# Kernel optimization log

Hardware: AMD Instinct MI355X
Metric: run time of the kernel (lower is better)

## Reference

```python
import jax, jax.numpy as jnp
import numpy as np

N_HEAD = 12
TOP_M = 16
MIN_SIZE = 2
MAX_SIZE = 8
ALPHA = 1.0
EPS = 1e-6

# Note: in the torch source, minimize_det=True and minimize_det=False select the
# identical subset (the sign flip in the score is exactly undone by flipping the
# comparisons), so we implement the single equivalent rule: maximize
# s = -log(det(K_S K_S^T) + 1e-6) / |S|**alpha.

def _token(qi, i, k_all, v_all):
    """Greedy DPP subset selection for one query token i. qi:[d], k_all/v_all:[T,d]."""
    T, d = k_all.shape
    slots = jnp.arange(MAX_SIZE)
    sim = k_all @ qi
    sim = jnp.where(jnp.arange(T) <= i, sim, -jnp.inf)  # causal mask
    vals, topidx = jax.lax.top_k(sim, TOP_M)
    avail0 = jnp.isfinite(vals) & (topidx != i)  # i is removed from candidates
    k_cand = k_all[topidx]                        # [M,d]
    cand_norm = jnp.sum(k_cand * k_cand, axis=-1)  # [M]
    ki = k_all[i]
    sel0 = jnp.zeros((MAX_SIZE,), jnp.int32).at[0].set(i.astype(jnp.int32))
    s0 = jax.lax.stop_gradient(-jnp.log(jnp.dot(ki, ki) + EPS))  # |S|=1 => size^alpha=1

    def body(state, _):
        sel, count, cur_s, avail, done = state
        # E: selected key vectors in slots < count, zeros elsewhere
        E = jnp.where((slots < count)[:, None], k_all[sel], 0.0)  # [S,d]
        G0 = E @ E.T                                              # [S,S]
        cross = k_cand @ E.T  # [M,S]; column `count` is 0 since that E row is 0
        u = (slots == count).astype(E.dtype)  # one-hot insertion slot
        # Gram of S u {c} for every candidate c, identity-padded beyond slot count
        grams = (G0[None]
                 + u[None, :, None] * cross[:, None, :]
                 + cross[:, :, None] * u[None, None, :]
                 + cand_norm[:, None, None] * (u[:, None] * u[None, :])[None])
        grams = grams + jnp.diag(jnp.where(slots > count, 1.0, 0.0))[None]
        det = jnp.linalg.det(grams.astype(jnp.float32))  # [M]
        s = -jnp.log(det + EPS) / (count + 1).astype(jnp.float32) ** ALPHA
        s = jax.lax.stop_gradient(jnp.where(avail, s, -jnp.inf))
        best = jnp.argmax(s)
        best_s = s[best]
        accept = (~done) & jnp.any(avail) & ((best_s > cur_s) | (count < MIN_SIZE))
        sel = jnp.where(accept & (slots == count), topidx[best].astype(jnp.int32), sel)
        avail = avail & ~(accept & (jnp.arange(TOP_M) == best))
        cur_s = jnp.where(accept, best_s, cur_s)
        count = count + accept.astype(count.dtype)
        done = done | ~accept
        return (sel, count, cur_s, avail, done), None

    init = (sel0, jnp.int32(1), s0, avail0, jnp.bool_(False))
    (sel, count, _, _, _), _ = jax.lax.scan(body, init, None, length=MAX_SIZE - 1)
    w = (slots < count).astype(v_all.dtype)
    return (v_all[sel] * w[:, None]).sum(0) / count.astype(v_all.dtype)

_tokens = jax.vmap(_token, in_axes=(0, 0, None, None))  # over T

def _head(qh, kh, vh):
    return _tokens(qh, jnp.arange(qh.shape[0]), kh, vh)

_attn = jax.vmap(jax.vmap(_head))  # over B, H

def _forward(x, W_attn, b_attn, W_proj, b_proj):
    B, T, C = x.shape
    hs = C // N_HEAD
    qkv = x @ W_attn + b_attn
    q, k, v = jnp.split(qkv, 3, axis=-1)
    q = q.reshape(B, T, N_HEAD, hs).transpose(0, 2, 1, 3)
    k = k.reshape(B, T, N_HEAD, hs).transpose(0, 2, 1, 3)
    v = v.reshape(B, T, N_HEAD, hs).transpose(0, 2, 1, 3)
    y = _attn(q, k, v)  # [B,H,T,hs]
    y = y.transpose(0, 2, 1, 3).reshape(B, T, C)
    return y @ W_proj + b_proj  # dropout=0.0 (eval)

def setup_inputs():
    key = jax.random.key(0)
    ks = jax.random.split(key, 3)
    B, T, C = 4, 512, 768
    return {
        "x": jax.random.normal(ks[0], (B, T, C), jnp.float32),
        "W_attn": jax.random.normal(ks[1], (C, 3 * C), jnp.float32) * 0.02,
        "b_attn": jnp.zeros((3 * C,), jnp.float32),
        "W_proj": jax.random.normal(ks[2], (C, C), jnp.float32) * 0.02,
        "b_proj": jnp.zeros((C,), jnp.float32),
    }

def reference(x, W_attn, b_attn, W_proj, b_proj):
    return _forward(x, W_attn, b_attn, W_proj, b_proj)
```

## Files before the change

### kernel.cpp

```cpp
#include <hip/hip_runtime.h>
#include <math.h>

constexpr int Bc = 4, Tc = 512, Cc = 768, Hc = 12, HSc = 64;
constexpr int QKVN = 3 * Cc;
constexpr double EPSd = 1e-6;

typedef unsigned short u16;
typedef __attribute__((ext_vector_type(8))) short short8;
typedef __attribute__((ext_vector_type(4))) float f32x4;

__device__ __forceinline__ u16 f2bf(float x) {
  unsigned u = __float_as_uint(x);
  return (u16)((u + 0x7FFFu + ((u >> 16) & 1u)) >> 16);
}
__device__ __forceinline__ float bf2f(u16 h) {
  return __uint_as_float((unsigned)h << 16);
}

__device__ __forceinline__ void gload16(const u16* g, u16* l) {
  __builtin_amdgcn_global_load_lds(
      (const __attribute__((address_space(1))) void*)g,
      (__attribute__((address_space(3))) void*)l, 16, 0, 0);
}

#define WAITVM0 asm volatile("s_waitcnt vmcnt(0)" ::: "memory")

__global__ void __launch_bounds__(256) convsplit3(
    const float* __restrict__ in, u16* __restrict__ H, u16* __restrict__ M,
    u16* __restrict__ L) {
  const int i = blockIdx.x * 256 + threadIdx.x;
  const float4 v = ((const float4*)in)[i];
  const float x[4] = {v.x, v.y, v.z, v.w};
  ushort4 hv, mv, lv;
  u16* hp = (u16*)&hv; u16* mp = (u16*)&mv; u16* lp = (u16*)&lv;
#pragma unroll
  for (int c = 0; c < 4; ++c) {
    const u16 h = f2bf(x[c]);
    const float r1 = x[c] - bf2f(h);
    const u16 m = f2bf(r1);
    const u16 l = f2bf(r1 - bf2f(m));
    hp[c] = h; mp[c] = m; lp[c] = l;
  }
  ((ushort4*)H)[i] = hv;
  ((ushort4*)M)[i] = mv;
  ((ushort4*)L)[i] = lv;
}

__global__ void __launch_bounds__(256) convsplit3_t(
    const float* __restrict__ W, u16* __restrict__ Th, u16* __restrict__ Tm,
    u16* __restrict__ Tl, int K, int Nn) {
  __shared__ float t[64][65];
  const int k0 = blockIdx.x * 64, n0 = blockIdx.y * 64;
#pragma unroll
  for (int u = 0; u < 16; ++u) {
    const int idx = u * 256 + threadIdx.x;
    const int r = idx >> 6, c = idx & 63;
    t[r][c] = W[(size_t)(k0 + r) * Nn + n0 + c];
  }
  __syncthreads();
#pragma unroll
  for (int u = 0; u < 16; ++u) {
    const int idx = u * 256 + threadIdx.x;
    const int n = idx >> 6, k = idx & 63;
    const float x = t[k][n];
    const u16 h = f2bf(x);
    const float r1 = x - bf2f(h);
    const u16 m = f2bf(r1);
    const u16 l = f2bf(r1 - bf2f(m));
    Th[(size_t)(n0 + n) * K + k0 + k] = h;
    Tm[(size_t)(n0 + n) * K + k0 + k] = m;
    Tl[(size_t)(n0 + n) * K + k0 + k] = l;
  }
}

template <bool WRITE_PARTIAL, int PLANES>
__global__ void __launch_bounds__(256, 3) gemm_mfma3(
    const u16* __restrict__ A, const u16* __restrict__ B,
    const float* __restrict__ bias, float* __restrict__ outp,
    int N, int kPerSplit, int strideA, int strideB) {
  __shared__ __align__(16) u16 AsF[2][PLANES * 64 * 32];
  __shared__ __align__(16) u16 BsF[2][PLANES * 64 * 32];
  const int tid = threadIdx.x;
  const int wid = tid >> 6;
  const int lane = tid & 63;
  const int lm = lane & 15, kg = lane >> 4;
  const int wr = wid >> 1, wc = wid & 1;
  const int rb = blockIdx.x * 64;
  const int cb = blockIdx.y * 64;
  const int kBeg = blockIdx.z * kPerSplit;

  const int trow = tid >> 2;
  const int tc4 = tid & 3;
  const int krot = ((tc4 - (trow >> 1)) & 3) * 8;
  const int sLds = tid * 8;
  int aOff = (rb + trow) * 768 + kBeg + krot;
  int bOff = (cb + trow) * 768 + kBeg + krot;

  f32x4 acc[2][2];
#pragma unroll
  for (int mf = 0; mf < 2; ++mf)
#pragma unroll
    for (int nf = 0; nf < 2; ++nf) acc[mf][nf] = (f32x4){0.f, 0.f, 0.f, 0.f};

  const int nIter = kPerSplit / 32;
  const int ckA = ((kg + (lm >> 1)) & 3) * 8;

  auto waitN = [&]() {
    if constexpr (PLANES == 3) {
      asm volatile("s_waitcnt vmcnt(6)" ::: "memory");
    } else {
      asm volatile("s_waitcnt vmcnt(4)" ::: "memory");
    }
  };
  auto stage = [&](int buf) {
#pragma unroll
    for (int p = 0; p < PLANES; ++p) {
      gload16(A + (size_t)p * strideA + aOff, &AsF[buf][p * 2048 + sLds]);
      gload16(B + (size_t)p * strideB + bOff, &BsF[buf][p * 2048 + sLds]);
    }
    aOff += 32; bOff += 32;
  };
  auto compute = [&](int buf) {
    short8 ah[2], am[2], al[2];
#pragma unroll
    for (int mf = 0; mf < 2; ++mf) {
      const int ro = (wr * 32 + mf * 16 + lm) * 32 + ckA;
      ah[mf] = *(const short8*)&AsF[buf][ro];
      am[mf] = *(const short8*)&AsF[buf][2048 + ro];
      if constexpr (PLANES == 3) al[mf] = *(const short8*)&AsF[buf][4096 + ro];
    }
#pragma unroll
    for (int nf = 0; nf < 2; ++nf) {
      const int co = (wc * 32 + nf * 16 + lm) * 32 + ckA;
      const short8 bh = *(const short8*)&BsF[buf][co];
      const short8 bm = *(const short8*)&BsF[buf][2048 + co];
      short8 bl;
      if constexpr (PLANES == 3) bl = *(const short8*)&BsF[buf][4096 + co];
#pragma unroll
      for (int mf = 0; mf < 2; ++mf) {
        if constexpr (PLANES == 3) {
          acc[mf][nf] = __builtin_amdgcn_mfma_f32_16x16x32_bf16(
              al[mf], bh, acc[mf][nf], 0, 0, 0);
          acc[mf][nf] = __builtin_amdgcn_mfma_f32_16x16x32_bf16(
              ah[mf], bl, acc[mf][nf], 0, 0, 0);
          acc[mf][nf] = __builtin_amdgcn_mfma_f32_16x16x32_bf16(
              am[mf], bm, acc[mf][nf], 0, 0, 0);
        }
        acc[mf][nf] = __builtin_amdgcn_mfma_f32_16x16x32_bf16(
            am[mf], bh, acc[mf][nf], 0, 0, 0);
        acc[mf][nf] = __builtin_amdgcn_mfma_f32_16x16x32_bf16(
            ah[mf], bm, acc[mf][nf], 0, 0, 0);
        acc[mf][nf] = __builtin_amdgcn_mfma_f32_16x16x32_bf16(
            ah[mf], bh, acc[mf][nf], 0, 0, 0);
      }
    }
  };

  stage(0);
  stage(1);
  for (int t = 0; t < nIter; t += 2) {
    if (t + 1 < nIter) { waitN(); } else { WAITVM0; }
    __builtin_amdgcn_s_barrier();
    compute(0);
    __builtin_amdgcn_s_barrier();
    if (t + 2 < nIter) stage(0);
    if (t + 2 < nIter) { waitN(); } else { WAITVM0; }
    __builtin_amdgcn_s_barrier();
    compute(1);
    __builtin_amdgcn_s_barrier();
    if (t + 3 < nIter) stage(1);
  }

  const int colb = cb + wc * 32 + lm;
  if (WRITE_PARTIAL) {
    float* Pp = outp + (size_t)blockIdx.z * 2048 * N;
#pragma unroll
    for (int mf = 0; mf < 2; ++mf)
#pragma unroll
      for (int r2 = 0; r2 < 4; ++r2) {
        float* orow =
            Pp + (size_t)(rb + wr * 32 + mf * 16 + kg * 4 + r2) * N + colb;
        orow[0]  = acc[mf][0][r2];
        orow[16] = acc[mf][1][r2];
      }
  } else {
    const float bb0 = bias[colb], bb1 = bias[colb + 16];
#pragma unroll
    for (int mf = 0; mf < 2; ++mf)
#pragma unroll
      for (int r2 = 0; r2 < 4; ++r2) {
        float* orow =
            outp + (size_t)(rb + wr * 32 + mf * 16 + kg * 4 + r2) * N + colb;
        orow[0]  = acc[mf][0][r2] + bb0;
        orow[16] = acc[mf][1][r2] + bb1;
      }
  }
}

__global__ void __launch_bounds__(256) reduce_bias_kernel(
    const float* __restrict__ P, const float* __restrict__ bias,
    float* __restrict__ outp, int MN, int N, int KS) {
  const int idx4 = (blockIdx.x * 256 + threadIdx.x) * 4;
  float4 acc = *(const float4*)&P[idx4];
  for (int ks = 1; ks < KS; ++ks) {
    const float4 p = *(const float4*)&P[(size_t)ks * MN + idx4];
    acc.x += p.x; acc.y += p.y; acc.z += p.z; acc.w += p.w;
  }
  const int col = idx4 % N;
  const float4 b4 = *(const float4*)&bias[col];
  acc.x += b4.x; acc.y += b4.y; acc.z += b4.z; acc.w += b4.w;
  *(float4*)&outp[idx4] = acc;
}

__global__ void __launch_bounds__(256) sims_kernel(
    const float* __restrict__ qkv, float* __restrict__ S) {
  const int bh = blockIdx.y;
  const int b = bh / Hc, h = bh % Hc;
  int it = 0;
  {
    const int t = blockIdx.x;
    while ((it + 1) * (it + 2) / 2 <= t) ++it;
  }
  const int jt = blockIdx.x - it * (it + 1) / 2;
  const int tid = threadIdx.x;
  const int tx = tid & 15, ty = tid >> 4;
  __shared__ float Qs[HSc][68];
  __shared__ float Ks[HSc][68];
  const float* base = qkv + (size_t)b * Tc * QKVN + h * HSc;
  {
    const int row = tid >> 2;
    const int d0 = (tid & 3) * 16;
    const float* qrow = base + (size_t)(it * 64 + row) * QKVN;
    const float* krow = base + (size_t)(jt * 64 + row) * QKVN + Cc;
#pragma unroll
    for (int u = 0; u < 4; ++u) {
      const float4 q4 = *(const float4*)&qrow[d0 + u * 4];
      const float4 k4 = *(const float4*)&krow[d0 + u * 4];
      Qs[d0 + u * 4 + 0][row] = q4.x; Qs[d0 + u * 4 + 1][row] = q4.y;
      Qs[d0 + u * 4 + 2][row] = q4.z; Qs[d0 + u * 4 + 3][row] = q4.w;
      Ks[d0 + u * 4 + 0][row] = k4.x; Ks[d0 + u * 4 + 1][row] = k4.y;
      Ks[d0 + u * 4 + 2][row] = k4.z; Ks[d0 + u * 4 + 3][row] = k4.w;
    }
  }
  __syncthreads();
  float acc[4][4];
#pragma unroll
  for (int m = 0; m < 4; ++m)
#pragma unroll
    for (int n = 0; n < 4; ++n) acc[m][n] = 0.0f;
#pragma unroll 4
  for (int d = 0; d < HSc; ++d) {
    const float4 a4 = *(const float4*)&Qs[d][ty * 4];
    const float4 b4 = *(const float4*)&Ks[d][tx * 4];
    const float a[4] = {a4.x, a4.y, a4.z, a4.w};
    const float bv[4] = {b4.x, b4.y, b4.z, b4.w};
#pragma unroll
    for (int m = 0; m < 4; ++m)
#pragma unroll
      for (int n = 0; n < 4; ++n) acc[m][n] += a[m] * bv[n];
  }
  float* Shead = S + (size_t)bh * Tc * Tc;
#pragma unroll
  for (int m = 0; m < 4; ++m) {
    const int i = it * 64 + ty * 4 + m;
    float4 o4 = {acc[m][0], acc[m][1], acc[m][2], acc[m][3]};
    *(float4*)&Shead[(size_t)i * Tc + jt * 64 + tx * 4] = o4;
  }
}

__global__ void __launch_bounds__(256) topk_kernel(
    const float* __restrict__ S, int* __restrict__ topidx,
    unsigned* __restrict__ availB) {
  const int tid = threadIdx.x;
  const int wv = tid >> 6, lane = tid & 63;
  const int tok = blockIdx.x * 4 + wv;
  const int i = tok & (Tc - 1);
  const float4* Sq = reinterpret_cast<const float4*>(S + (size_t)tok * Tc);
  unsigned long long key[8];
#pragma unroll
  for (int r = 0; r < 2; ++r) {
    const int jb = lane * 8 + r * 4;
    if (jb <= i) {
      const float4 v4 = Sq[lane * 2 + r];
      const float vv[4] = {v4.x, v4.y, v4.z, v4.w};
#pragma unroll
      for (int c = 0; c < 4; ++c) {
        const int j = jb + c;
        const unsigned u = __float_as_uint(vv[c]);
        const unsigned s = (u & 0x80000000u) ? ~u : (u | 0x80000000u);
        key[r * 4 + c] = (j <= i)
            ? (((unsigned long long)s << 32) | (unsigned)(511 - j))
            : 0ull;
      }
    } else {
      key[r * 4 + 0] = 0ull; key[r * 4 + 1] = 0ull;
      key[r * 4 + 2] = 0ull; key[r * 4 + 3] = 0ull;
    }
  }
#define CE8(a, b)                                                   \
  {                                                                 \
    const unsigned long long lo_ = key[a] < key[b] ? key[a] : key[b]; \
    const unsigned long long hi_ = key[a] < key[b] ? key[b] : key[a]; \
    key[a] = hi_; key[b] = lo_;                                     \
  }
  CE8(0, 1) CE8(2, 3) CE8(0, 2) CE8(1, 3) CE8(1, 2)
  CE8(4, 5) CE8(6, 7) CE8(4, 6) CE8(5, 7) CE8(5, 6)
  CE8(0, 4) CE8(1, 5) CE8(2, 6) CE8(3, 7)
  CE8(2, 4) CE8(3, 5)
  CE8(1, 2) CE8(3, 4) CE8(5, 6)
#undef CE8

  unsigned avail = 0;
#pragma unroll
  for (int m = 0; m < 16; ++m) {
    unsigned g = (unsigned)(key[0] >> 32);
    const unsigned myhi = g;
#pragma unroll
    for (int msk = 1; msk <= 32; msk <<= 1) {
      const unsigned o = __shfl_xor(g, msk);
      g = o > g ? o : g;
    }
    const unsigned long long ball = __ballot(myhi == g);
    const int winner = __ffsll((unsigned long long)ball) - 1;
    const unsigned lo = __shfl((unsigned)key[0], winner);
    const int j = 511 - (int)lo;
    if (lane == 0) topidx[(size_t)tok * 16 + m] = j & 511;
    if (g > 0x007FFFFFu && j != i) avail |= (1u << m);
    if (lane == winner) {
      key[0] = key[1]; key[1] = key[2]; key[2] = key[3]; key[3] = key[4];
      key[4] = key[5]; key[5] = key[6]; key[6] = key[7]; key[7] = 0ull;
    }
  }
  if (lane == 0) availB[tok] = avail;
}

__global__ void __launch_bounds__(256, 4) select_kernel(
    const float* __restrict__ qkv, const int* __restrict__ topidx,
    const unsigned* __restrict__ availB, u16* __restrict__ yh,
    u16* __restrict__ ym) {
  const int tid = threadIdx.x;
  const int wv = tid >> 6, lane = tid & 63;
  const int half = lane >> 5;
  const int l32 = lane & 31;
  const int m = l32 >> 1;
  const int q = l32 & 1;
  const int hbase = half << 5;

  const int tok = blockIdx.x * 8 + wv * 2 + half;
  const int bh = tok >> 9;
  const int i = tok & (Tc - 1);
  const int b = bh / Hc;
  const int h = bh % Hc;

  const float* base = qkv + (size_t)b * Tc * QKVN + h * HSc;
  const float* kbase = base + Cc;
  const float* vbase = base + 2 * Cc;

  const int tidx = topidx[(size_t)tok * 16 + m];
  unsigned avail = availB[tok];

  float kreg[32], kireg[32];
  {
    const float* kc = kbase + (size_t)tidx * QKVN + q * 32;
    const float* ki = kbase + (size_t)i * QKVN + q * 32;
#pragma unroll
    for (int u = 0; u < 8; ++u) {
      const float4 c4 = *(const float4*)&kc[u * 4];
      const float4 i4 = *(const float4*)&ki[u * 4];
      kreg[u * 4 + 0] = c4.x; kreg[u * 4 + 1] = c4.y;
      kreg[u * 4 + 2] = c4.z; kreg[u * 4 + 3] = c4.w;
      kireg[u * 4 + 0] = i4.x; kireg[u * 4 + 1] = i4.y;
      kireg[u * 4 + 2] = i4.z; kireg[u * 4 + 3] = i4.w;
    }
  }
  float cnorm_f = 0.0f, c0_f = 0.0f, kii_f = 0.0f;
#pragma unroll
  for (int e = 0; e < 32; ++e) {
    cnorm_f += kreg[e] * kreg[e];
    c0_f += kreg[e] * kireg[e];
    kii_f += kireg[e] * kireg[e];
  }
  cnorm_f += __shfl_xor(cnorm_f, 1);
  c0_f += __shfl_xor(c0_f, 1);
  kii_f += __shfl_xor(kii_f, 1);

  const double kii = (double)kii_f;
  double z[8];
#pragma unroll
  for (int t = 0; t < 8; ++t) z[t] = 0.0;
  z[0] = (double)c0_f / sqrt(kii);
  double schur = (double)cnorm_f - z[0] * z[0];
  double detS = kii;
  double Dprev = 0.0;
  int count = 1;
  int sel[8];
  sel[0] = i;
#pragma unroll
  for (int a = 1; a < 8; ++a) sel[a] = 0;
  bool hdone = false;

#pragma unroll
  for (int it = 0; it < 7; ++it) {
    const double D = detS * schur + EPSd;
    const bool act = ((avail >> m) & 1u) != 0;
    const bool bad = !(D > 0.0);
    double dkey = act ? (bad ? -INFINITY : D) : INFINITY;
    int bm = m;
#pragma unroll
    for (int msk = 2; msk <= 16; msk <<= 1) {
      const double ok2 = __shfl_xor(dkey, msk);
      const int om = __shfl_xor(bm, msk);
      const bool t2 = (ok2 < dkey) || (ok2 == dkey && om < bm);
      dkey = t2 ? ok2 : dkey;
      bm = t2 ? om : bm;
    }
    const double Dbest = __shfl(D, hbase | (bm * 2));
    bool acc_ok;
    if (it == 0) {
      acc_ok = true;
    } else {
      double pA = Dbest, pB = Dprev;
#pragma unroll
      for (int j = 0; j < it; ++j) pA *= Dbest;
#pragma unroll
      for (int j = 0; j < it + 1; ++j) pB *= Dprev;
      acc_ok = ((avail >> bm) & 1u) && (Dbest >= 0.0) && (Dprev >= 0.0) &&
               (pA < pB);
    }
    const bool X = !hdone && (avail != 0u) && acc_ok;
    hdone = hdone || !X;
    if (X) {
      float cp_f = 0.0f;
#pragma unroll
      for (int e = 0; e < 32; ++e) {
        const float kb = __shfl(kreg[e], hbase | (bm * 2) | q);
        cp_f += kreg[e] * kb;
      }
      cp_f += __shfl_xor(cp_f, 1);
      const double schur_b = __shfl(schur, hbase | (bm * 2));
      double sum = 0.0;
#pragma unroll
      for (int t = 0; t <= it; ++t) {
        const double zbt = __shfl(z[t], hbase | (bm * 2));
        sum += z[t] * zbt;
      }
      const double znew = ((double)cp_f - sum) / sqrt(schur_b);
      z[it + 1] = znew;
      schur -= znew * znew;
      detS *= schur_b;
      Dprev = Dbest;
      avail &= ~(1u << bm);
      ++count;
      sel[it + 1] = __shfl(tidx, hbase | (bm * 2));
    }
    if (__all(hdone)) break;
  }

  double acc0 = 0.0, acc1 = 0.0;
#pragma unroll
  for (int a = 0; a < 8; ++a)
    if (a < count) {
      const float* vrow = vbase + (size_t)sel[a] * QKVN;
      acc0 += (double)vrow[l32];
      acc1 += (double)vrow[l32 + 32];
    }
  const float v0 = (float)(acc0 / (double)count);
  const float v1 = (float)(acc1 / (double)count);
  const size_t yidx = (((size_t)b * Tc + i) * Hc + h) * HSc + l32;
  {
    const u16 hv = f2bf(v0);
    yh[yidx] = hv; ym[yidx] = f2bf(v0 - bf2f(hv));
  }
  {
    const u16 hv = f2bf(v1);
    yh[yidx + 32] = hv; ym[yidx + 32] = f2bf(v1 - bf2f(hv));
  }
}

extern "C" void kernel_launch(void* const* d_in, const int* in_sizes, int n_in,
                              void* d_out, int out_size, void* d_ws, size_t ws_size,
                              hipStream_t stream) {
  (void)in_sizes; (void)n_in; (void)out_size; (void)ws_size;
  const float* x  = (const float*)d_in[0];
  const float* Wa = (const float*)d_in[1];
  const float* ba = (const float*)d_in[2];
  const float* Wp = (const float*)d_in[3];
  const float* bp = (const float*)d_in[4];
  float* out = (float*)d_out;

  constexpr size_t XPLANE = (size_t)Bc * Tc * Cc;
  constexpr size_t WAPLANE = (size_t)QKVN * Cc;
  constexpr size_t WPPLANE = (size_t)Cc * Cc;

  float* qkv = (float*)d_ws;
  int* topidx = (int*)(qkv + (size_t)Bc * Tc * QKVN);
  unsigned* availB = (unsigned*)(topidx + (size_t)Bc * Hc * Tc * 16);
  float* regionB = (float*)(availB + (size_t)Bc * Hc * Tc);
  float* S = regionB;
  float* Pproj = regionB;
  u16* Xh = (u16*)regionB;
  u16* Wath = Xh + 3 * XPLANE;
  u16* Wpth = (u16*)(regionB + (size_t)3 * 2048 * Cc);
  u16* yhp = Wpth + 3 * WPPLANE;

  const int MNproj = Bc * Tc * Cc;

  hipLaunchKernelGGL(convsplit3, dim3(1536), dim3(256), 0, stream,
                     x, Xh, Xh + XPLANE, Xh + 2 * XPLANE);
  hipLaunchKernelGGL(convsplit3_t, dim3(12, 36), dim3(256), 0, stream,
                     Wa, Wath, Wath + WAPLANE, Wath + 2 * WAPLANE, Cc, QKVN);
  hipLaunchKernelGGL((gemm_mfma3<false, 3>), dim3(32, QKVN / 64, 1),
                     dim3(256), 0, stream, Xh, Wath, ba, qkv, QKVN, Cc,
                     (int)XPLANE, (int)WAPLANE);
  hipLaunchKernelGGL(sims_kernel, dim3(36, Bc * Hc), dim3(256), 0,
                     stream, qkv, S);
  hipLaunchKernelGGL(topk_kernel, dim3(Bc * Hc * Tc / 4), dim3(256), 0,
                     stream, S, topidx, availB);
  hipLaunchKernelGGL(select_kernel, dim3(Bc * Hc * Tc / 8), dim3(256), 0,
                     stream, qkv, topidx, availB, yhp, yhp + XPLANE);
  hipLaunchKernelGGL(convsplit3_t, dim3(12, 12), dim3(256), 0, stream,
                     Wp, Wpth, Wpth + WPPLANE, Wpth + 2 * WPPLANE, Cc, Cc);
  hipLaunchKernelGGL((gemm_mfma3<true, 2>), dim3(32, Cc / 64, 3), dim3(256),
                     0, stream, yhp, Wpth, nullptr, Pproj, Cc, 256,
                     (int)XPLANE, (int)WPPLANE);
  hipLaunchKernelGGL(reduce_bias_kernel, dim3(MNproj / 1024), dim3(256), 0,
                     stream, Pproj, bp, out, MNproj, Cc, 3);
}
```

Measured before the change: 252.6 us.

## Map one lane per candidate in select kernel, 16 tokens per block

```diff
diff --git a/kernel.cpp b/kernel.cpp
--- a/kernel.cpp
+++ b/kernel.cpp
@@ -334,19 +334,16 @@
   if (lane == 0) availB[tok] = avail;
 }
 
-__global__ void __launch_bounds__(256, 4) select_kernel(
+__global__ void __launch_bounds__(256, 3) select_kernel(
     const float* __restrict__ qkv, const int* __restrict__ topidx,
     const unsigned* __restrict__ availB, u16* __restrict__ yh,
     u16* __restrict__ ym) {
   const int tid = threadIdx.x;
-  const int wv = tid >> 6, lane = tid & 63;
-  const int half = lane >> 5;
-  const int l32 = lane & 31;
-  const int m = l32 >> 1;
-  const int q = l32 & 1;
-  const int hbase = half << 5;
-
-  const int tok = blockIdx.x * 8 + wv * 2 + half;
+  const int lane = tid & 63;
+  const int m = lane & 15;
+  const int gbase = lane & 48;
+
+  const int tok = blockIdx.x * 16 + (tid >> 4);
   const int bh = tok >> 9;
   const int i = tok & (Tc - 1);
   const int b = bh / Hc;
@@ -359,30 +356,26 @@
   const int tidx = topidx[(size_t)tok * 16 + m];
   unsigned avail = availB[tok];
 
-  float kreg[32], kireg[32];
+  float kreg[64];
+  float cnorm_f = 0.0f, c0_f = 0.0f, kii_f = 0.0f;
   {
-    const float* kc = kbase + (size_t)tidx * QKVN + q * 32;
-    const float* ki = kbase + (size_t)i * QKVN + q * 32;
-#pragma unroll
-    for (int u = 0; u < 8; ++u) {
+    const float* kc = kbase + (size_t)tidx * QKVN;
+    const float* ki = kbase + (size_t)i * QKVN;
+#pragma unroll
+    for (int u = 0; u < 16; ++u) {
       const float4 c4 = *(const float4*)&kc[u * 4];
       const float4 i4 = *(const float4*)&ki[u * 4];
-      kreg[u * 4 + 0] = c4.x; kreg[u * 4 + 1] = c4.y;
-      kreg[u * 4 + 2] = c4.z; kreg[u * 4 + 3] = c4.w;
-      kireg[u * 4 + 0] = i4.x; kireg[u * 4 + 1] = i4.y;
-      kireg[u * 4 + 2] = i4.z; kireg[u * 4 + 3] = i4.w;
-    }
-  }
-  float cnorm_f = 0.0f, c0_f = 0.0f, kii_f = 0.0f;
-#pragma unroll
-  for (int e = 0; e < 32; ++e) {
-    cnorm_f += kreg[e] * kreg[e];
-    c0_f += kreg[e] * kireg[e];
-    kii_f += kireg[e] * kireg[e];
-  }
-  cnorm_f += __shfl_xor(cnorm_f, 1);
-  c0_f += __shfl_xor(c0_f, 1);
-  kii_f += __shfl_xor(kii_f, 1);
+      const float cv[4] = {c4.x, c4.y, c4.z, c4.w};
+      const float iv[4] = {i4.x, i4.y, i4.z, i4.w};
+#pragma unroll
+      for (int c = 0; c < 4; ++c) {
+        kreg[u * 4 + c] = cv[c];
+        cnorm_f += cv[c] * cv[c];
+        c0_f += cv[c] * iv[c];
+        kii_f += iv[c] * iv[c];
+      }
+    }
+  }
 
   const double kii = (double)kii_f;
   double z[8];
@@ -397,7 +390,7 @@
   sel[0] = i;
 #pragma unroll
   for (int a = 1; a < 8; ++a) sel[a] = 0;
-  bool hdone = false;
+  bool gdone = false;
 
 #pragma unroll
   for (int it = 0; it < 7; ++it) {
@@ -407,14 +400,14 @@
     double dkey = act ? (bad ? -INFINITY : D) : INFINITY;
     int bm = m;
 #pragma unroll
-    for (int msk = 2; msk <= 16; msk <<= 1) {
+    for (int msk = 1; msk <= 8; msk <<= 1) {
       const double ok2 = __shfl_xor(dkey, msk);
       const int om = __shfl_xor(bm, msk);
       const bool t2 = (ok2 < dkey) || (ok2 == dkey && om < bm);
       dkey = t2 ? ok2 : dkey;
       bm = t2 ? om : bm;
     }
-    const double Dbest = __shfl(D, hbase | (bm * 2));
+    const double Dbest = __shfl(D, gbase + bm);
     bool acc_ok;
     if (it == 0) {
       acc_ok = true;
@@ -427,21 +420,20 @@
       acc_ok = ((avail >> bm) & 1u) && (Dbest >= 0.0) && (Dprev >= 0.0) &&
                (pA < pB);
     }
-    const bool X = !hdone && (avail != 0u) && acc_ok;
-    hdone = hdone || !X;
+    const bool X = !gdone && (avail != 0u) && acc_ok;
+    gdone = gdone || !X;
     if (X) {
       float cp_f = 0.0f;
 #pragma unroll
-      for (int e = 0; e < 32; ++e) {
-        const float kb = __shfl(kreg[e], hbase | (bm * 2) | q);
+      for (int e = 0; e < 64; ++e) {
+        const float kb = __shfl(kreg[e], gbase + bm);
         cp_f += kreg[e] * kb;
       }
-      cp_f += __shfl_xor(cp_f, 1);
-      const double schur_b = __shfl(schur, hbase | (bm * 2));
+      const double schur_b = __shfl(schur, gbase + bm);
       double sum = 0.0;
 #pragma unroll
       for (int t = 0; t <= it; ++t) {
-        const double zbt = __shfl(z[t], hbase | (bm * 2));
+        const double zbt = __shfl(z[t], gbase + bm);
         sum += z[t] * zbt;
       }
       const double znew = ((double)cp_f - sum) / sqrt(schur_b);
@@ -451,30 +443,33 @@
       Dprev = Dbest;
       avail &= ~(1u << bm);
       ++count;
-      sel[it + 1] = __shfl(tidx, hbase | (bm * 2));
-    }
-    if (__all(hdone)) break;
-  }
-
-  double acc0 = 0.0, acc1 = 0.0;
+      sel[it + 1] = __shfl(tidx, gbase + bm);
+    }
+    if (__all(gdone)) break;
+  }
+
+  double a0 = 0.0, a1 = 0.0, a2 = 0.0, a3 = 0.0;
 #pragma unroll
   for (int a = 0; a < 8; ++a)
     if (a < count) {
-      const float* vrow = vbase + (size_t)sel[a] * QKVN;
-      acc0 += (double)vrow[l32];
-      acc1 += (double)vrow[l32 + 32];
-    }
-  const float v0 = (float)(acc0 / (double)count);
-  const float v1 = (float)(acc1 / (double)count);
-  const size_t yidx = (((size_t)b * Tc + i) * Hc + h) * HSc + l32;
-  {
-    const u16 hv = f2bf(v0);
-    yh[yidx] = hv; ym[yidx] = f2bf(v0 - bf2f(hv));
-  }
-  {
-    const u16 hv = f2bf(v1);
-    yh[yidx + 32] = hv; ym[yidx + 32] = f2bf(v1 - bf2f(hv));
-  }
+      const float4 v4 = *(const float4*)&vbase[(size_t)sel[a] * QKVN + m * 4];
+      a0 += (double)v4.x; a1 += (double)v4.y;
+      a2 += (double)v4.z; a3 += (double)v4.w;
+    }
+  const double cd = (double)count;
+  const float vo[4] = {(float)(a0 / cd), (float)(a1 / cd),
+                       (float)(a2 / cd), (float)(a3 / cd)};
+  const size_t yidx = (((size_t)b * Tc + i) * Hc + h) * HSc + m * 4;
+  ushort4 hv4, mv4;
+  u16* hp = (u16*)&hv4; u16* mp = (u16*)&mv4;
+#pragma unroll
+  for (int c = 0; c < 4; ++c) {
+    const u16 hv = f2bf(vo[c]);
+    hp[c] = hv;
+    mp[c] = f2bf(vo[c] - bf2f(hv));
+  }
+  *(ushort4*)&yh[yidx] = hv4;
+  *(ushort4*)&ym[yidx] = mv4;
 }
 
 extern "C" void kernel_launch(void* const* d_in, const int* in_sizes, int n_in,
@@ -516,7 +511,7 @@
                      stream, qkv, S);
   hipLaunchKernelGGL(topk_kernel, dim3(Bc * Hc * Tc / 4), dim3(256), 0,
                      stream, S, topidx, availB);
-  hipLaunchKernelGGL(select_kernel, dim3(Bc * Hc * Tc / 8), dim3(256), 0,
+  hipLaunchKernelGGL(select_kernel, dim3(Bc * Hc * Tc / 16), dim3(256), 0,
                      stream, qkv, topidx, availB, yhp, yhp + XPLANE);
   hipLaunchKernelGGL(convsplit3_t, dim3(12, 12), dim3(256), 0, stream,
                      Wp, Wpth, Wpth + WPPLANE, Wpth + 2 * WPPLANE, Cc, Cc);
```

Result: slower. 258.7 us (+2.4%).
